# Optimization experiments

Hardware: AMD Instinct MI355X
Metric: run time of the kernel (lower is better)

Reference implementation:

```python
import jax, jax.numpy as jnp
import numpy as np

# MoE_Bottleneck constants from source
E = 4   # number of experts
K = 2   # top-k routing


def setup_inputs() -> dict:
    key = jax.random.key(0)
    ks = jax.random.split(key, 10)
    B, C1, H, W = 8, 256, 64, 64
    C2 = 256
    Ch = C2 // 2  # c_ = int(c2*0.5) = 128
    x = jax.random.normal(ks[0], (B, C1, H, W), dtype=jnp.float32)
    # Conv = conv2d(no bias)+BN+SiLU; BN folded into weight scale + bias (eval mode).
    W1 = jax.random.normal(ks[1], (Ch, C1), dtype=jnp.float32) / np.sqrt(C1)
    b1 = jax.random.normal(ks[2], (Ch,), dtype=jnp.float32) * 0.1
    Wr = jax.random.normal(ks[3], (E, Ch), dtype=jnp.float32) / np.sqrt(Ch)
    br = jax.random.normal(ks[4], (E,), dtype=jnp.float32) * 0.1
    # Expert Conv(c_, c_, 3, 1): full 3x3 kernels [E, Cout, Cin, 3, 3]
    We = jax.random.normal(ks[5], (E, Ch, Ch, 3, 3), dtype=jnp.float32) / np.sqrt(Ch * 9)
    be = jax.random.normal(ks[6], (E, Ch), dtype=jnp.float32) * 0.1
    W3 = jax.random.normal(ks[7], (C2, Ch), dtype=jnp.float32) / np.sqrt(Ch)
    b3 = jax.random.normal(ks[8], (C2,), dtype=jnp.float32) * 0.1
    return {"x": x, "W1": W1, "b1": b1, "Wr": Wr, "br": br,
            "We": We, "be": be, "W3": W3, "b3": b3}


def reference(x, W1, b1, Wr, br, We, be, W3, b3):
    silu = jax.nn.silu
    # conv1: 1x1 conv + (folded BN) + SiLU
    x_in = silu(jnp.einsum('bchw,oc->bohw', x, W1) + b1[None, :, None, None])
    B, C, H, Wd = x_in.shape
    N = B * H * Wd
    xr = x_in.transpose(0, 2, 3, 1).reshape(N, C)            # [N, C] tokens
    # router: 1x1 conv -> per-pixel logits over E experts
    logits = xr @ Wr.T + br                                   # [N, E]
    probs = jax.nn.softmax(logits, axis=-1)
    topw, topi = jax.lax.top_k(probs, K)                      # [N, K]
    topw = topw / jnp.sum(topw, axis=-1, keepdims=True)       # renormalize top-k
    # dense [N, E] routing-weight matrix (indices within a row are unique)
    wmat = jnp.zeros_like(probs).at[jnp.arange(N)[:, None], topi].set(topw)
    # Experts: 3x3 conv applied to 1x1 spatial patches with pad=1 -> only the
    # center tap We[..., 1, 1] contributes (padding is zeros). Folded-BN bias + SiLU.
    Wc = We[:, :, :, 1, 1]                                    # [E, Cout, Cin]
    eout = silu(jnp.einsum('nc,eoc->neo', xr, Wc) + be[None]) # [N, E, C]
    moe = jnp.einsum('neo,ne->no', eout, wmat)                # weighted combine
    out = moe.reshape(B, H, Wd, C).transpose(0, 3, 1, 2)
    # conv3: 1x1 conv + SiLU
    y = silu(jnp.einsum('bchw,oc->bohw', out, W3) + b3[None, :, None, None])
    # shortcut=True and c1 == c2
    return y + x
```

## Files before the change

kernel.cpp:

```cpp
#include <hip/hip_runtime.h>
#include <hip/hip_bf16.h>


typedef unsigned short u16;
typedef unsigned int   u32;
typedef __attribute__((ext_vector_type(8))) short short8;
typedef __attribute__((ext_vector_type(4))) float f32x4;

#define MFMA16 __builtin_amdgcn_mfma_f32_16x16x32_bf16

__device__ __forceinline__ float silu_f(float v) { return v / (1.0f + __expf(-v)); }
__device__ __forceinline__ u16 f2bf(float f) {
    u32 u = __float_as_uint(f);
    return (u16)((u + 0x7fff + ((u >> 16) & 1)) >> 16);
}
__device__ __forceinline__ float bf2f(u16 h) { return __uint_as_float(((u32)h) << 16); }
__device__ __forceinline__ u32 pkbf(float a, float b) {
    __hip_bfloat162 h2 = __float22bfloat162_rn(make_float2(a, b));
    u32 r; __builtin_memcpy(&r, &h2, 4); return r;
}

__global__ void prep_weights(const float* __restrict__ W1,
                             const float* __restrict__ We,
                             const float* __restrict__ W3,
                             u16* __restrict__ ws)
{
    int idx = blockIdx.x * 256 + threadIdx.x;
    if (idx < 36864) {
        int kc = idx / 9216, r = idx % 9216;
        int n = r / 72, j = r % 72;
        float v = (j < 64) ? W1[n * 256 + kc * 64 + j] : 0.0f;
        u16 h = f2bf(v);
        float lo = v - bf2f(h);
        ws[idx] = h;
        ws[36864 + idx] = f2bf(lo);
    } else if (idx < 106496) {
        int i = idx - 36864;
        int e = i / 17408, r = i % 17408;
        int n = r / 136, j = r % 136;
        ws[73728 + i] = (j < 128)
            ? f2bf(We[(size_t)(((e * 128 + n) * 128 + j) * 9) + 4]) : (u16)0;
    } else if (idx < 141312) {
        int i = idx - 106496;
        int h = i / 17408, r = i % 17408;
        int n = r / 136, j = r % 136;
        ws[143360 + i] = (j < 128)
            ? f2bf(W3[(size_t)(h * 128 + n) * 128 + j]) : (u16)0;
    }
}

__device__ __forceinline__ void dma_u16(const u16* __restrict__ g, u16* l, int i, int tid) {
    int idx = i * 256 + tid;
    int ub  = i * 256 + (tid & 192);
    __builtin_amdgcn_global_load_lds(g + (size_t)idx * 8, l + ub * 8, 16, 0, 0);
}

__global__ __launch_bounds__(256, 2)
void fused_moe_mfma(const float* __restrict__ x,
                    const float* __restrict__ b1,
                    const float* __restrict__ Wr,
                    const float* __restrict__ br,
                    const float* __restrict__ be,
                    const float* __restrict__ b3,
                    const u16* __restrict__ wbf,
                    float* __restrict__ out)
{
    __shared__ __align__(16) unsigned char smem[71680];
    u16*   const sWhi = (u16*)(smem);
    u16*   const sWlo = (u16*)(smem + 18432);
    u16*   const sAhi = (u16*)(smem + 36864);
    u16*   const sAlo = (u16*)(smem + 46080);
    u16*   const sA2  = (u16*)(smem);
    u16*   const sWe  = (u16*)(smem + 17408);
    u16*   const sA3  = (u16*)(smem + 52224);
    u16*   const sW3  = (u16*)(smem + 17408);
    float* const sY   = (float*)(smem);
    float* const sWr  = (float*)(smem + 69632);

    const int tid = threadIdx.x;
    const int l  = tid & 63;
    const int w  = tid >> 6;
    const int lr = l & 15;
    const int g  = l >> 4;
    const int lk = g * 8;
    const int mrow = 16 * w + 4 * g;

    const int n0  = blockIdx.x << 6;
    const float* xb = x   + ((size_t)(n0 >> 12) * 256) * 4096 + (n0 & 4095);
    float*       ob = out + ((size_t)(n0 >> 12) * 256) * 4096 + (n0 & 4095);

    if (tid < 128) *(float4*)&sWr[tid * 4] = *(const float4*)&Wr[tid * 4];

    f32x4 acc1[8];
#pragma unroll
    for (int f = 0; f < 8; ++f) acc1[f] = (f32x4){0.f, 0.f, 0.f, 0.f};

    const int c2a = tid >> 4;
    const int c2b = 16 + c2a;
    const int m4  = (tid & 15) << 2;

#pragma unroll 1
    for (int kc = 0; kc < 4; ++kc) {
        __syncthreads();
        const float* xa0 = xb + (size_t)(kc * 64 + 2 * c2a) * 4096 + m4;
        const float* xa1 = xb + (size_t)(kc * 64 + 2 * c2b) * 4096 + m4;
        float4 fa0 = *(const float4*)xa0;
        float4 fb0 = *(const float4*)(xa0 + 4096);
        float4 fa1 = *(const float4*)xa1;
        float4 fb1 = *(const float4*)(xa1 + 4096);
#pragma unroll
        for (int i = 0; i < 5; ++i) {
            if (i * 256 + tid < 1152) {
                dma_u16(wbf + (size_t)kc * 9216,           sWhi, i, tid);
                dma_u16(wbf + (size_t)(36864 + kc * 9216), sWlo, i, tid);
            }
        }
        u32* H = (u32*)sAhi; u32* L = (u32*)sAlo;
        {
            float fav[4] = {fa0.x, fa0.y, fa0.z, fa0.w};
            float fbv[4] = {fb0.x, fb0.y, fb0.z, fb0.w};
#pragma unroll
            for (int r = 0; r < 4; ++r) {
                int ui = (m4 + r) * 36 + c2a;
                u32 hi = pkbf(fav[r], fbv[r]);
                float la = fav[r] - __uint_as_float(hi << 16);
                float lb = fbv[r] - __uint_as_float(hi & 0xffff0000u);
                H[ui] = hi; L[ui] = pkbf(la, lb);
            }
        }
        {
            float fav[4] = {fa1.x, fa1.y, fa1.z, fa1.w};
            float fbv[4] = {fb1.x, fb1.y, fb1.z, fb1.w};
#pragma unroll
            for (int r = 0; r < 4; ++r) {
                int ui = (m4 + r) * 36 + c2b;
                u32 hi = pkbf(fav[r], fbv[r]);
                float la = fav[r] - __uint_as_float(hi << 16);
                float lb = fbv[r] - __uint_as_float(hi & 0xffff0000u);
                H[ui] = hi; L[ui] = pkbf(la, lb);
            }
        }
        __syncthreads();
#pragma unroll
        for (int ks = 0; ks < 2; ++ks) {
            short8 ah = *(const short8*)&sAhi[(16 * w + lr) * 72 + ks * 32 + lk];
            short8 al = *(const short8*)&sAlo[(16 * w + lr) * 72 + ks * 32 + lk];
#pragma unroll
            for (int f = 0; f < 8; ++f) {
                int bo = (16 * f + lr) * 72 + ks * 32 + lk;
                short8 bh = *(const short8*)&sWhi[bo];
                short8 bl = *(const short8*)&sWlo[bo];
                acc1[f] = MFMA16(ah, bh, acc1[f], 0, 0, 0);
                acc1[f] = MFMA16(al, bh, acc1[f], 0, 0, 0);
                acc1[f] = MFMA16(ah, bl, acc1[f], 0, 0, 0);
                acc1[f] = MFMA16(al, bl, acc1[f], 0, 0, 0);
            }
        }
    }
    __syncthreads();

    float xin[8][4];
#pragma unroll
    for (int f = 0; f < 8; ++f) {
        float bias = b1[16 * f + lr];
#pragma unroll
        for (int i = 0; i < 4; ++i) xin[f][i] = silu_f(acc1[f][i] + bias);
    }
#pragma unroll
    for (int f = 0; f < 8; ++f) {
        int c = 16 * f + lr;
#pragma unroll
        for (int i = 0; i < 4; ++i)
            sA2[(mrow + i) * 136 + c] = f2bf(xin[f][i]);
    }

    float lg[4][4];
#pragma unroll
    for (int e = 0; e < 4; ++e)
#pragma unroll
        for (int i = 0; i < 4; ++i) lg[e][i] = 0.f;
#pragma unroll
    for (int f = 0; f < 8; ++f) {
        int c = 16 * f + lr;
        float w0 = sWr[c], w1 = sWr[128 + c], w2 = sWr[256 + c], w3 = sWr[384 + c];
#pragma unroll
        for (int i = 0; i < 4; ++i) {
            float xv = xin[f][i];
            lg[0][i] += xv * w0; lg[1][i] += xv * w1;
            lg[2][i] += xv * w2; lg[3][i] += xv * w3;
        }
    }
#pragma unroll
    for (int d = 1; d < 16; d <<= 1)
#pragma unroll
        for (int e = 0; e < 4; ++e)
#pragma unroll
            for (int i = 0; i < 4; ++i)
                lg[e][i] += __shfl_xor(lg[e][i], d, 64);

    float br0 = br[0], br1 = br[1], br2 = br[2], br3 = br[3];
    float rw[4][4];
#pragma unroll
    for (int i = 0; i < 4; ++i) {
        float le0 = lg[0][i] + br0, le1 = lg[1][i] + br1;
        float le2 = lg[2][i] + br2, le3 = lg[3][i] + br3;
        int c0 = (le1 > le0) + (le2 > le0) + (le3 > le0);
        int c1 = (le0 >= le1) + (le2 > le1) + (le3 > le1);
        int c2 = (le0 >= le2) + (le1 >= le2) + (le3 > le2);
        int c3 = (le0 >= le3) + (le1 >= le3) + (le2 >= le3);
        float m = fmaxf(fmaxf(le0, le1), fmaxf(le2, le3));
        float p0 = (c0 < 2) ? __expf(le0 - m) : 0.f;
        float p1 = (c1 < 2) ? __expf(le1 - m) : 0.f;
        float p2 = (c2 < 2) ? __expf(le2 - m) : 0.f;
        float p3 = (c3 < 2) ? __expf(le3 - m) : 0.f;
        float inv = 1.0f / (p0 + p1 + p2 + p3);
        rw[0][i] = p0 * inv; rw[1][i] = p1 * inv;
        rw[2][i] = p2 * inv; rw[3][i] = p3 * inv;
    }

    f32x4 macc[8];
#pragma unroll
    for (int f = 0; f < 8; ++f) macc[f] = (f32x4){0.f, 0.f, 0.f, 0.f};

#pragma unroll 1
    for (int e = 0; e < 4; ++e) {
        __syncthreads();
#pragma unroll
        for (int i9 = 0; i9 < 9; ++i9)
            if (i9 * 256 + tid < 2176)
                dma_u16(wbf + (size_t)(73728 + e * 17408), sWe, i9, tid);
        __syncthreads();
        f32x4 acce[8];
#pragma unroll
        for (int f = 0; f < 8; ++f) acce[f] = (f32x4){0.f, 0.f, 0.f, 0.f};
#pragma unroll
        for (int ks = 0; ks < 4; ++ks) {
            short8 a = *(const short8*)&sA2[(16 * w + lr) * 136 + ks * 32 + lk];
#pragma unroll
            for (int f = 0; f < 8; ++f) {
                short8 bb = *(const short8*)&sWe[(16 * f + lr) * 136 + ks * 32 + lk];
                acce[f] = MFMA16(a, bb, acce[f], 0, 0, 0);
            }
        }
#pragma unroll
        for (int f = 0; f < 8; ++f) {
            float bias = be[e * 128 + 16 * f + lr];
#pragma unroll
            for (int i = 0; i < 4; ++i)
                macc[f][i] += rw[e][i] * silu_f(acce[f][i] + bias);
        }
    }
#pragma unroll
    for (int f = 0; f < 8; ++f) {
        int c = 16 * f + lr;
#pragma unroll
        for (int i = 0; i < 4; ++i)
            sA3[(mrow + i) * 136 + c] = f2bf(macc[f][i]);
    }

#pragma unroll 1
    for (int h = 0; h < 2; ++h) {
        __syncthreads();
#pragma unroll
        for (int i9 = 0; i9 < 9; ++i9)
            if (i9 * 256 + tid < 2176)
                dma_u16(wbf + (size_t)(143360 + h * 17408), sW3, i9, tid);
        __syncthreads();
        f32x4 acc3[8];
#pragma unroll
        for (int f = 0; f < 8; ++f) acc3[f] = (f32x4){0.f, 0.f, 0.f, 0.f};
#pragma unroll
        for (int ks = 0; ks < 4; ++ks) {
            short8 a = *(const short8*)&sA3[(16 * w + lr) * 136 + ks * 32 + lk];
#pragma unroll
            for (int f = 0; f < 8; ++f) {
                short8 bb = *(const short8*)&sW3[(16 * f + lr) * 136 + ks * 32 + lk];
                acc3[f] = MFMA16(a, bb, acc3[f], 0, 0, 0);
            }
        }
        __syncthreads();
#pragma unroll
        for (int f = 0; f < 8; ++f) {
            int o = 16 * f + lr;
            float bias = b3[h * 128 + o];
#pragma unroll
            for (int i = 0; i < 4; ++i)
                sY[o * 68 + mrow + i] = silu_f(acc3[f][i] + bias);
        }
        __syncthreads();
#pragma unroll
        for (int q = 0; q < 8; ++q) {
            int idx = q * 256 + tid;
            int o = idx >> 4, mq = (idx & 15) << 2;
            int og = h * 128 + o;
            float4 vy = *(float4*)&sY[o * 68 + mq];
            float4 r  = *(const float4*)&xb[(size_t)og * 4096 + mq];
            vy.x += r.x; vy.y += r.y; vy.z += r.z; vy.w += r.w;
            *(float4*)&ob[(size_t)og * 4096 + mq] = vy;
        }
    }
}

extern "C" void kernel_launch(void* const* d_in, const int* in_sizes, int n_in,
                              void* d_out, int out_size, void* d_ws, size_t ws_size,
                              hipStream_t stream)
{
    const float* x  = (const float*)d_in[0];
    const float* W1 = (const float*)d_in[1];
    const float* b1 = (const float*)d_in[2];
    const float* Wr = (const float*)d_in[3];
    const float* br = (const float*)d_in[4];
    const float* We = (const float*)d_in[5];
    const float* be = (const float*)d_in[6];
    const float* W3 = (const float*)d_in[7];
    const float* b3 = (const float*)d_in[8];
    float* outp = (float*)d_out;
    u16* wbf = (u16*)d_ws;

    hipLaunchKernelGGL(prep_weights, dim3(552), dim3(256), 0, stream,
                       W1, We, W3, wbf);
    hipLaunchKernelGGL(fused_moe_mfma, dim3(512), dim3(256), 0, stream,
                       x, b1, Wr, br, be, b3, wbf, outp);
}
```

Baseline: 57.87 us.

## Double-buffer expert and conv3 weight staging with XOR-swizzled unpadded LDS layout

Expert and conv3 weights are stored in bf16 with an XOR-swizzled, unpadded 128-column layout. Two LDS buffers let the next weight chunk load asynchronously while the current chunk's MFMAs run, replacing the old load-then-sync before each expert and conv3 half. The output staging buffer is also swizzled for float4 writes, and router weights are now read from global memory instead of LDS. LDS use grows to 80KB per block, which may limit how many blocks fit on a CU.

```diff
diff --git a/kernel.cpp b/kernel.cpp
--- a/kernel.cpp
+++ b/kernel.cpp
@@ -19,6 +19,7 @@
     __hip_bfloat162 h2 = __float22bfloat162_rn(make_float2(a, b));
     u32 r; __builtin_memcpy(&r, &h2, 4); return r;
 }
+__device__ __forceinline__ int swzkey(int row) { return (row ^ (row >> 2)) & 7; }
 
 __global__ void prep_weights(const float* __restrict__ W1,
                              const float* __restrict__ We,
@@ -34,21 +35,31 @@
         float lo = v - bf2f(h);
         ws[idx] = h;
         ws[36864 + idx] = f2bf(lo);
-    } else if (idx < 106496) {
+    } else if (idx < 102400) {
         int i = idx - 36864;
-        int e = i / 17408, r = i % 17408;
-        int n = r / 136, j = r % 136;
-        ws[73728 + i] = (j < 128)
-            ? f2bf(We[(size_t)(((e * 128 + n) * 128 + j) * 9) + 4]) : (u16)0;
-    } else if (idx < 141312) {
-        int i = idx - 106496;
-        int h = i / 17408, r = i % 17408;
-        int n = r / 136, j = r % 136;
-        ws[143360 + i] = (j < 128)
-            ? f2bf(W3[(size_t)(h * 128 + n) * 128 + j]) : (u16)0;
-    }
-}
-
+        int e = i >> 14, r = i & 16383;
+        int o = r >> 7, rem = r & 127;
+        int ps = rem >> 3, t = rem & 7;
+        int gi = (ps & 8) | ((ps ^ swzkey(o)) & 7);
+        int c = gi * 8 + t;
+        ws[73728 + i] = f2bf(We[(size_t)(((e * 128 + o) * 128 + c) * 9) + 4]);
+    } else if (idx < 135168) {
+        int i = idx - 102400;
+        int h = i >> 14, r = i & 16383;
+        int o = r >> 7, rem = r & 127;
+        int ps = rem >> 3, t = rem & 7;
+        int gi = (ps & 8) | ((ps ^ swzkey(o)) & 7);
+        int c = gi * 8 + t;
+        ws[139264 + i] = f2bf(W3[(size_t)(h * 128 + o) * 128 + c]);
+    }
+}
+
+__device__ __forceinline__ void stage_chunk(const u16* __restrict__ g, u16* l, int tid) {
+#pragma unroll
+    for (int i = 0; i < 8; ++i)
+        __builtin_amdgcn_global_load_lds(g + (size_t)(i * 256 + tid) * 8,
+                                         l + (size_t)(i * 256 + (tid & 192)) * 8, 16, 0, 0);
+}
 __device__ __forceinline__ void dma_u16(const u16* __restrict__ g, u16* l, int i, int tid) {
     int idx = i * 256 + tid;
     int ub  = i * 256 + (tid & 192);
@@ -58,24 +69,22 @@
 __global__ __launch_bounds__(256, 2)
 void fused_moe_mfma(const float* __restrict__ x,
                     const float* __restrict__ b1,
-                    const float* __restrict__ Wr,
+                    const float* __restrict__ Wrg,
                     const float* __restrict__ br,
                     const float* __restrict__ be,
                     const float* __restrict__ b3,
                     const u16* __restrict__ wbf,
                     float* __restrict__ out)
 {
-    __shared__ __align__(16) unsigned char smem[71680];
+    __shared__ __align__(16) unsigned char smem[81920];
     u16*   const sWhi = (u16*)(smem);
     u16*   const sWlo = (u16*)(smem + 18432);
     u16*   const sAhi = (u16*)(smem + 36864);
     u16*   const sAlo = (u16*)(smem + 46080);
-    u16*   const sA2  = (u16*)(smem);
-    u16*   const sWe  = (u16*)(smem + 17408);
-    u16*   const sA3  = (u16*)(smem + 52224);
-    u16*   const sW3  = (u16*)(smem + 17408);
-    float* const sY   = (float*)(smem);
-    float* const sWr  = (float*)(smem + 69632);
+    u16*   const A2   = (u16*)(smem);
+    u16*   const bufA = (u16*)(smem + 16384);
+    u16*   const bufB = (u16*)(smem + 49152);
+    float* const sY   = (float*)(smem + 16384);
 
     const int tid = threadIdx.x;
     const int l  = tid & 63;
@@ -84,12 +93,15 @@
     const int g  = l >> 4;
     const int lk = g * 8;
     const int mrow = 16 * w + 4 * g;
+    const int arow = 16 * w + lr;
+    const int akey = swzkey(arow);
+    int okey[8];
+#pragma unroll
+    for (int f = 0; f < 8; ++f) okey[f] = swzkey(16 * f + lr);
 
     const int n0  = blockIdx.x << 6;
     const float* xb = x   + ((size_t)(n0 >> 12) * 256) * 4096 + (n0 & 4095);
     float*       ob = out + ((size_t)(n0 >> 12) * 256) * 4096 + (n0 & 4095);
-
-    if (tid < 128) *(float4*)&sWr[tid * 4] = *(const float4*)&Wr[tid * 4];
 
     f32x4 acc1[8];
 #pragma unroll
@@ -159,6 +171,9 @@
     }
     __syncthreads();
 
+    stage_chunk(wbf + 73728,         bufA, tid);
+    stage_chunk(wbf + 73728 + 16384, bufB, tid);
+
     float xin[8][4];
 #pragma unroll
     for (int f = 0; f < 8; ++f) {
@@ -168,10 +183,13 @@
     }
 #pragma unroll
     for (int f = 0; f < 8; ++f) {
-        int c = 16 * f + lr;
-#pragma unroll
-        for (int i = 0; i < 4; ++i)
-            sA2[(mrow + i) * 136 + c] = f2bf(xin[f][i]);
+        int c = 16 * f + lr, gi = c >> 3;
+#pragma unroll
+        for (int i = 0; i < 4; ++i) {
+            int m = mrow + i;
+            int ps = (gi & 8) | ((gi ^ swzkey(m)) & 7);
+            A2[m * 128 + ps * 8 + (c & 7)] = f2bf(xin[f][i]);
+        }
     }
 
     float lg[4][4];
@@ -182,7 +200,7 @@
 #pragma unroll
     for (int f = 0; f < 8; ++f) {
         int c = 16 * f + lr;
-        float w0 = sWr[c], w1 = sWr[128 + c], w2 = sWr[256 + c], w3 = sWr[384 + c];
+        float w0 = Wrg[c], w1 = Wrg[128 + c], w2 = Wrg[256 + c], w3 = Wrg[384 + c];
 #pragma unroll
         for (int i = 0; i < 4; ++i) {
             float xv = xin[f][i];
@@ -217,6 +235,7 @@
         rw[0][i] = p0 * inv; rw[1][i] = p1 * inv;
         rw[2][i] = p2 * inv; rw[3][i] = p3 * inv;
     }
+    __syncthreads();
 
     f32x4 macc[8];
 #pragma unroll
@@ -224,21 +243,19 @@
 
 #pragma unroll 1
     for (int e = 0; e < 4; ++e) {
-        __syncthreads();
-#pragma unroll
-        for (int i9 = 0; i9 < 9; ++i9)
-            if (i9 * 256 + tid < 2176)
-                dma_u16(wbf + (size_t)(73728 + e * 17408), sWe, i9, tid);
-        __syncthreads();
+        const u16* Wb = (e & 1) ? bufB : bufA;
         f32x4 acce[8];
 #pragma unroll
         for (int f = 0; f < 8; ++f) acce[f] = (f32x4){0.f, 0.f, 0.f, 0.f};
 #pragma unroll
         for (int ks = 0; ks < 4; ++ks) {
-            short8 a = *(const short8*)&sA2[(16 * w + lr) * 136 + ks * 32 + lk];
+            int gi = ks * 4 + g;
+            int psA = (gi & 8) | ((gi ^ akey) & 7);
+            short8 a = *(const short8*)&A2[arow * 128 + psA * 8];
 #pragma unroll
             for (int f = 0; f < 8; ++f) {
-                short8 bb = *(const short8*)&sWe[(16 * f + lr) * 136 + ks * 32 + lk];
+                int psB = (gi & 8) | ((gi ^ okey[f]) & 7);
+                short8 bb = *(const short8*)&Wb[(16 * f + lr) * 128 + psB * 8];
                 acce[f] = MFMA16(a, bb, acce[f], 0, 0, 0);
             }
         }
@@ -249,55 +266,69 @@
             for (int i = 0; i < 4; ++i)
                 macc[f][i] += rw[e][i] * silu_f(acce[f][i] + bias);
         }
-    }
+        __syncthreads();
+        if (e < 2)      stage_chunk(wbf + 73728 + (e + 2) * 16384, (e & 1) ? bufB : bufA, tid);
+        else if (e == 2) stage_chunk(wbf + 139264,                 bufA, tid);
+        else              ;
+    }
+
 #pragma unroll
     for (int f = 0; f < 8; ++f) {
-        int c = 16 * f + lr;
-#pragma unroll
-        for (int i = 0; i < 4; ++i)
-            sA3[(mrow + i) * 136 + c] = f2bf(macc[f][i]);
-    }
+        int c = 16 * f + lr, gi = c >> 3;
+#pragma unroll
+        for (int i = 0; i < 4; ++i) {
+            int m = mrow + i;
+            int ps = (gi & 8) | ((gi ^ swzkey(m)) & 7);
+            A2[m * 128 + ps * 8 + (c & 7)] = f2bf(macc[f][i]);
+        }
+    }
+    __syncthreads();
+    stage_chunk(wbf + 139264 + 16384, bufB, tid);
 
 #pragma unroll 1
     for (int h = 0; h < 2; ++h) {
-        __syncthreads();
-#pragma unroll
-        for (int i9 = 0; i9 < 9; ++i9)
-            if (i9 * 256 + tid < 2176)
-                dma_u16(wbf + (size_t)(143360 + h * 17408), sW3, i9, tid);
-        __syncthreads();
+        const u16* Wb = h ? bufB : bufA;
         f32x4 acc3[8];
 #pragma unroll
         for (int f = 0; f < 8; ++f) acc3[f] = (f32x4){0.f, 0.f, 0.f, 0.f};
 #pragma unroll
         for (int ks = 0; ks < 4; ++ks) {
-            short8 a = *(const short8*)&sA3[(16 * w + lr) * 136 + ks * 32 + lk];
+            int gi = ks * 4 + g;
+            int psA = (gi & 8) | ((gi ^ akey) & 7);
+            short8 a = *(const short8*)&A2[arow * 128 + psA * 8];
 #pragma unroll
             for (int f = 0; f < 8; ++f) {
-                short8 bb = *(const short8*)&sW3[(16 * f + lr) * 136 + ks * 32 + lk];
+                int psB = (gi & 8) | ((gi ^ okey[f]) & 7);
+                short8 bb = *(const short8*)&Wb[(16 * f + lr) * 128 + psB * 8];
                 acc3[f] = MFMA16(a, bb, acc3[f], 0, 0, 0);
             }
         }
         __syncthreads();
+        int mg = mrow >> 2;
 #pragma unroll
         for (int f = 0; f < 8; ++f) {
             int o = 16 * f + lr;
             float bias = b3[h * 128 + o];
-#pragma unroll
-            for (int i = 0; i < 4; ++i)
-                sY[o * 68 + mrow + i] = silu_f(acc3[f][i] + bias);
+            float4 v;
+            v.x = silu_f(acc3[f][0] + bias);
+            v.y = silu_f(acc3[f][1] + bias);
+            v.z = silu_f(acc3[f][2] + bias);
+            v.w = silu_f(acc3[f][3] + bias);
+            *(float4*)&sY[o * 64 + ((mg ^ okey[f]) << 2)] = v;
         }
         __syncthreads();
 #pragma unroll
         for (int q = 0; q < 8; ++q) {
             int idx = q * 256 + tid;
-            int o = idx >> 4, mq = (idx & 15) << 2;
+            int o = idx >> 4, mq = idx & 15;
             int og = h * 128 + o;
-            float4 vy = *(float4*)&sY[o * 68 + mq];
-            float4 r  = *(const float4*)&xb[(size_t)og * 4096 + mq];
+            float4 vy = *(const float4*)&sY[o * 64 + ((mq ^ swzkey(o)) << 2)];
+            size_t goff = (size_t)og * 4096 + (mq << 2);
+            float4 r = *(const float4*)&xb[goff];
             vy.x += r.x; vy.y += r.y; vy.z += r.z; vy.w += r.w;
-            *(float4*)&ob[(size_t)og * 4096 + mq] = vy;
-        }
+            *(float4*)&ob[goff] = vy;
+        }
+        if (h == 0) __syncthreads();
     }
 }
 
@@ -317,7 +348,7 @@
     float* outp = (float*)d_out;
     u16* wbf = (u16*)d_ws;
 
-    hipLaunchKernelGGL(prep_weights, dim3(552), dim3(256), 0, stream,
+    hipLaunchKernelGGL(prep_weights, dim3(528), dim3(256), 0, stream,
                        W1, We, W3, wbf);
     hipLaunchKernelGGL(fused_moe_mfma, dim3(512), dim3(256), 0, stream,
                        x, b1, Wr, br, be, b3, wbf, outp);
```

Result: faster. 54.31 us (-6.2%).
